# Kernel tuning notes

Measured on AMD Instinct MI355X. Metric: run time of the kernel, lower is better.

Reference implementation:

```python
import jax, jax.numpy as jnp
import numpy as np

ALPHA = 0.0005625
R_TIA = 0.1
DENOM = 2.0 * 1.5 * 0.025  # 2*n*VT = 0.075
V_D = 0.1
BN_EPS = 1e-5
KSZ, STRIDE, PAD = 3, 1, 1


def _unfold(x, k, s, p):
    # torch F.unfold equivalent: (N, C*k*k, L), channel-major then (ki, kj)
    N, C, H, W = x.shape
    Ho = (H + 2 * p - k) // s + 1
    Wo = (W + 2 * p - k) // s + 1
    xp = jnp.pad(x, ((0, 0), (0, 0), (p, p), (p, p)))
    cols = [xp[:, :, i:i + s * Ho:s, j:j + s * Wo:s]
            for i in range(k) for j in range(k)]  # each (N, C, Ho, Wo)
    patches = jnp.stack(cols, axis=2)             # (N, C, k*k, Ho, Wo)
    return patches.reshape(N, C * k * k, Ho * Wo), Ho, Wo


def setup_inputs() -> dict:
    key = jax.random.key(0)
    kx, kt = jax.random.split(key)
    x = jax.random.normal(kx, (32, 3, 32, 32), dtype=jnp.float32)
    theta = jax.random.uniform(kt, (3 * KSZ * KSZ, 64), dtype=jnp.float32,
                               minval=0.0, maxval=9.0)
    gamma = jnp.ones((64,), dtype=jnp.float32)
    beta = jnp.zeros((64,), dtype=jnp.float32)
    return {"x": x, "theta": theta, "gamma": gamma, "beta": beta}


def reference(x, theta, gamma, beta):
    N = x.shape[0]
    C_out = theta.shape[1]
    patches, Ho, Wo = _unfold(x, KSZ, STRIDE, PAD)      # (N, K, L)
    V_j = patches.transpose(0, 2, 1)[..., None]          # (N, L, K, 1)
    t1 = jax.nn.softplus((V_j - theta) / DENOM) ** 2     # (N, L, K, Cout)
    t2 = jax.nn.softplus((V_j - theta - V_D) / DENOM) ** 2
    I_k = ALPHA * jnp.sum(t1 - t2, axis=2)               # (N, L, Cout)
    V_out = (I_k * R_TIA).transpose(0, 2, 1).reshape(N, C_out, Ho, Wo)
    # BatchNorm2d in training mode: biased batch statistics
    mean = V_out.mean(axis=(0, 2, 3), keepdims=True)
    var = V_out.var(axis=(0, 2, 3), keepdims=True)
    V_hat = (V_out - mean) * jax.lax.rsqrt(var + BN_EPS)
    return V_hat * gamma[None, :, None, None] + beta[None, :, None, None]
```

## Files before the change

### kernel.cpp

```cpp
#include <hip/hip_runtime.h>


constexpr float INV_D  = 13.333333333333334f;
constexpr float C_NEG  = 0.2635971381157267f;
constexpr double OUT_SC = 5.625e-5 * 0.48045301391820142;
constexpr int   NCHUNK = 512;

__global__ __launch_bounds__(256)
void nlc_compute(const float* __restrict__ x, const float* __restrict__ theta,
                 float* __restrict__ vout, float* __restrict__ psum,
                 float* __restrict__ psq)
{
    __shared__ alignas(16) float thc[27 * 16];
    const int tid   = threadIdx.x;
    const int chunk = blockIdx.x >> 2;
    const int cbase = (blockIdx.x & 3) * 16;

    for (int i = tid; i < 27 * 16; i += 256) {
        const int k = i >> 4, cc = i & 15;
        thc[i] = __expf(-theta[k * 64 + cbase + cc] * INV_D);
    }
    __syncthreads();

    const int lane = tid & 63;
    const int wv   = tid >> 6;
    const int p    = chunk * 64 + lane;
    const int n    = p >> 10;
    const int hw   = p & 1023;
    const int h    = hw >> 5;
    const int w    = hw & 31;

    const float* xn = x + n * 3072;
    const float4* thv4 = reinterpret_cast<const float4*>(thc);

    int ad[9];
    unsigned okm = 0;
#pragma unroll
    for (int ki = 0; ki < 3; ++ki) {
#pragma unroll
        for (int kj = 0; kj < 3; ++kj) {
            const int  hh = h + ki - 1;
            const int  ww = w + kj - 1;
            const bool ok = ((unsigned)hh < 32u) & ((unsigned)ww < 32u);
            ad[ki * 3 + kj] = ok ? (hh * 32 + ww) : 0;
            okm |= (unsigned)ok << (ki * 3 + kj);
        }
    }

    float acc0 = 0.f, acc1 = 0.f, acc2 = 0.f, acc3 = 0.f;

#pragma unroll 1
    for (int ci = 0; ci < 3; ++ci) {
        float Ev[9];
#pragma unroll
        for (int j = 0; j < 9; ++j) {
            const float xv  = xn[ci * 1024 + ad[j]];
            const float val = ((okm >> j) & 1u) ? xv : 0.0f;
            Ev[j] = fminf(__expf(val * INV_D), 3.0e38f);
        }
#pragma unroll
        for (int j = 0; j < 9; ++j) {
            const float4 t4 = thv4[(ci * 9 + j) * 4 + wv];
            {
                const float E  = Ev[j] * t4.x;
                const float l1 = __log2f(1.0f + E);
                const float l2 = __log2f(fmaf(E, C_NEG, 1.0f));
                acc0 = fmaf(l1, l1, acc0);
                acc0 = fmaf(-l2, l2, acc0);
            }
            {
                const float E  = Ev[j] * t4.y;
                const float l1 = __log2f(1.0f + E);
                const float l2 = __log2f(fmaf(E, C_NEG, 1.0f));
                acc1 = fmaf(l1, l1, acc1);
                acc1 = fmaf(-l2, l2, acc1);
            }
            {
                const float E  = Ev[j] * t4.z;
                const float l1 = __log2f(1.0f + E);
                const float l2 = __log2f(fmaf(E, C_NEG, 1.0f));
                acc2 = fmaf(l1, l1, acc2);
                acc2 = fmaf(-l2, l2, acc2);
            }
            {
                const float E  = Ev[j] * t4.w;
                const float l1 = __log2f(1.0f + E);
                const float l2 = __log2f(fmaf(E, C_NEG, 1.0f));
                acc3 = fmaf(l1, l1, acc3);
                acc3 = fmaf(-l2, l2, acc3);
            }
        }
    }

    const float acc[4] = {acc0, acc1, acc2, acc3};
#pragma unroll
    for (int i = 0; i < 4; ++i) {
        const int   c  = cbase + wv * 4 + i;
        const float vo = acc[i];
        vout[(n << 16) + (c << 10) + hw] = vo;

        float s = vo, q = vo * vo;
#pragma unroll
        for (int off = 32; off > 0; off >>= 1) {
            s += __shfl_xor(s, off, 64);
            q += __shfl_xor(q, off, 64);
        }
        if (lane == 0) {
            psum[c * NCHUNK + chunk] = s;
            psq [c * NCHUNK + chunk] = q;
        }
    }
}

__global__ __launch_bounds__(256)
void nlc_finish(const float* __restrict__ psum, const float* __restrict__ psq,
                const float* __restrict__ gamma, const float* __restrict__ beta,
                float* __restrict__ vout)
{
    const int b   = blockIdx.x;
    const int c   = b >> 3;
    const int seg = b & 7;
    const int tid = threadIdx.x;

    float4* p0 = reinterpret_cast<float4*>(vout)
               + ((seg * 4 + 0) * 64 + c) * 256 + tid;
    float4* p1 = p0 + 64 * 256;
    float4* p2 = p1 + 64 * 256;
    float4* p3 = p2 + 64 * 256;
    float4 v0 = *p0, v1 = *p1, v2 = *p2, v3 = *p3;

    double s = (double)psum[c * NCHUNK + tid] + (double)psum[c * NCHUNK + 256 + tid];
    double q = (double)psq [c * NCHUNK + tid] + (double)psq [c * NCHUNK + 256 + tid];
#pragma unroll
    for (int off = 32; off > 0; off >>= 1) {
        s += __shfl_xor(s, off, 64);
        q += __shfl_xor(q, off, 64);
    }
    __shared__ double ls[4], lq[4];
    __shared__ float  scsh[2];
    if ((tid & 63) == 0) { ls[tid >> 6] = s; lq[tid >> 6] = q; }
    __syncthreads();
    if (tid == 0) {
        s = ls[0] + ls[1] + ls[2] + ls[3];
        q = lq[0] + lq[1] + lq[2] + lq[3];
        const double inv    = 1.0 / 32768.0;
        const double mean_a = s * inv;
        const double var_a  = q * inv - mean_a * mean_a;
        const double var_V  = var_a * OUT_SC * OUT_SC;
        const double rstd   = 1.0 / sqrt(var_V + 1e-5);
        const double sc     = (double)gamma[c] * rstd * OUT_SC;
        const double sh     = (double)beta[c] - mean_a * sc;
        scsh[0] = (float)sc;
        scsh[1] = (float)sh;
    }
    __syncthreads();
    const float sc = scsh[0];
    const float sh = scsh[1];

#define NLC_BN4(v) \
    v.x = fmaf(v.x, sc, sh); v.y = fmaf(v.y, sc, sh); \
    v.z = fmaf(v.z, sc, sh); v.w = fmaf(v.w, sc, sh);
    NLC_BN4(v0) NLC_BN4(v1) NLC_BN4(v2) NLC_BN4(v3)
#undef NLC_BN4

    *p0 = v0; *p1 = v1; *p2 = v2; *p3 = v3;
}

extern "C" void kernel_launch(void* const* d_in, const int* in_sizes, int n_in,
                              void* d_out, int out_size, void* d_ws, size_t ws_size,
                              hipStream_t stream)
{
    const float* x     = (const float*)d_in[0];
    const float* theta = (const float*)d_in[1];
    const float* gamma = (const float*)d_in[2];
    const float* beta  = (const float*)d_in[3];
    float* out = (float*)d_out;

    float* psum = (float*)d_ws;
    float* psq  = psum + 64 * NCHUNK;

    nlc_compute<<<NCHUNK * 4, 256, 0, stream>>>(x, theta, out, psum, psq);
    nlc_finish <<<512, 256, 0, stream>>>(psum, psq, gamma, beta, out);
}
```

Before: 33.79 us.

## Precompute input exponentials and use cubic series when whole wave has small E

Adds a small prepass kernel that computes exp(x/D) once per input element, so the conv kernel loads precomputed values instead of recomputing the exponential nine times per pixel. In the main loop, when every lane of a wave has E below a threshold, the two log2-squared terms are replaced by a cubic Taylor polynomial, skipping the transcendental calls. Theta in [0,9] makes E mostly tiny, so the fast branch should be taken often. The cost is an extra kernel launch, a workspace buffer, wave-uniform branches, and a small approximation error below the threshold.

```diff
diff --git a/kernel.cpp b/kernel.cpp
--- a/kernel.cpp
+++ b/kernel.cpp
@@ -2,12 +2,29 @@
 
 
 constexpr float INV_D  = 13.333333333333334f;
-constexpr float C_NEG  = 0.2635971381157267f;
-constexpr double OUT_SC = 5.625e-5 * 0.48045301391820142;
+constexpr double CD    = 0.26359713811572677;
+constexpr float C_NEG  = (float)CD;
+constexpr double LN2SQ = 0.4804530139182014;
+constexpr double OUT_SC = 5.625e-5 * LN2SQ;
+constexpr float TA = (float)((1.0 - CD * CD) / LN2SQ);
+constexpr float TB = (float)((1.0 - CD * CD * CD) / LN2SQ);
+constexpr float E_THR = 0.125f;
 constexpr int   NCHUNK = 512;
 
 __global__ __launch_bounds__(256)
-void nlc_compute(const float* __restrict__ x, const float* __restrict__ theta,
+void nlc_exp(const float* __restrict__ x, float* __restrict__ xe)
+{
+    const int i = blockIdx.x * 256 + threadIdx.x;
+    float4 v = reinterpret_cast<const float4*>(x)[i];
+    v.x = fminf(__expf(v.x * INV_D), 3.0e38f);
+    v.y = fminf(__expf(v.y * INV_D), 3.0e38f);
+    v.z = fminf(__expf(v.z * INV_D), 3.0e38f);
+    v.w = fminf(__expf(v.w * INV_D), 3.0e38f);
+    reinterpret_cast<float4*>(xe)[i] = v;
+}
+
+__global__ __launch_bounds__(256)
+void nlc_compute(const float* __restrict__ xe, const float* __restrict__ theta,
                  float* __restrict__ vout, float* __restrict__ psum,
                  float* __restrict__ psq)
 {
@@ -30,7 +47,7 @@
     const int h    = hw >> 5;
     const int w    = hw & 31;
 
-    const float* xn = x + n * 3072;
+    const float* xn = xe + n * 3072;
     const float4* thv4 = reinterpret_cast<const float4*>(thc);
 
     int ad[9];
@@ -54,38 +71,46 @@
         float Ev[9];
 #pragma unroll
         for (int j = 0; j < 9; ++j) {
-            const float xv  = xn[ci * 1024 + ad[j]];
-            const float val = ((okm >> j) & 1u) ? xv : 0.0f;
-            Ev[j] = fminf(__expf(val * INV_D), 3.0e38f);
+            const float ev = xn[ci * 1024 + ad[j]];
+            Ev[j] = ((okm >> j) & 1u) ? ev : 1.0f;
         }
 #pragma unroll
         for (int j = 0; j < 9; ++j) {
             const float4 t4 = thv4[(ci * 9 + j) * 4 + wv];
-            {
-                const float E  = Ev[j] * t4.x;
-                const float l1 = __log2f(1.0f + E);
-                const float l2 = __log2f(fmaf(E, C_NEG, 1.0f));
+            const float E0 = Ev[j] * t4.x;
+            const float E1 = Ev[j] * t4.y;
+            const float E2 = Ev[j] * t4.z;
+            const float E3 = Ev[j] * t4.w;
+
+            if (__all(E0 <= E_THR)) {
+                acc0 = fmaf(E0 * E0, fmaf(-TB, E0, TA), acc0);
+            } else {
+                const float l1 = __log2f(1.0f + E0);
+                const float l2 = __log2f(fmaf(E0, C_NEG, 1.0f));
                 acc0 = fmaf(l1, l1, acc0);
                 acc0 = fmaf(-l2, l2, acc0);
             }
-            {
-                const float E  = Ev[j] * t4.y;
-                const float l1 = __log2f(1.0f + E);
-                const float l2 = __log2f(fmaf(E, C_NEG, 1.0f));
+            if (__all(E1 <= E_THR)) {
+                acc1 = fmaf(E1 * E1, fmaf(-TB, E1, TA), acc1);
+            } else {
+                const float l1 = __log2f(1.0f + E1);
+                const float l2 = __log2f(fmaf(E1, C_NEG, 1.0f));
                 acc1 = fmaf(l1, l1, acc1);
                 acc1 = fmaf(-l2, l2, acc1);
             }
-            {
-                const float E  = Ev[j] * t4.z;
-                const float l1 = __log2f(1.0f + E);
-                const float l2 = __log2f(fmaf(E, C_NEG, 1.0f));
+            if (__all(E2 <= E_THR)) {
+                acc2 = fmaf(E2 * E2, fmaf(-TB, E2, TA), acc2);
+            } else {
+                const float l1 = __log2f(1.0f + E2);
+                const float l2 = __log2f(fmaf(E2, C_NEG, 1.0f));
                 acc2 = fmaf(l1, l1, acc2);
                 acc2 = fmaf(-l2, l2, acc2);
             }
-            {
-                const float E  = Ev[j] * t4.w;
-                const float l1 = __log2f(1.0f + E);
-                const float l2 = __log2f(fmaf(E, C_NEG, 1.0f));
+            if (__all(E3 <= E_THR)) {
+                acc3 = fmaf(E3 * E3, fmaf(-TB, E3, TA), acc3);
+            } else {
+                const float l1 = __log2f(1.0f + E3);
+                const float l2 = __log2f(fmaf(E3, C_NEG, 1.0f));
                 acc3 = fmaf(l1, l1, acc3);
                 acc3 = fmaf(-l2, l2, acc3);
             }
@@ -178,7 +203,9 @@
 
     float* psum = (float*)d_ws;
     float* psq  = psum + 64 * NCHUNK;
-
-    nlc_compute<<<NCHUNK * 4, 256, 0, stream>>>(x, theta, out, psum, psq);
+    float* xe   = psq  + 64 * NCHUNK;
+
+    nlc_exp    <<<96, 256, 0, stream>>>(x, xe);
+    nlc_compute<<<NCHUNK * 4, 256, 0, stream>>>(xe, theta, out, psum, psq);
     nlc_finish <<<512, 256, 0, stream>>>(psum, psq, gamma, beta, out);
 }
```

Measured after the change: 33.63 us. About the same (-0.5%).

## Precompute exp(x) and exp(-theta) in prepass kernels; two channels per wave

Applied to the files above, without the earlier changes.

Adds two small prepass kernels that compute exp(x/D) for the input and exp(-theta/D) per channel into workspace. The main kernel then loads these directly and reads theta terms as wave-uniform scalars, with no shared-memory staging or __syncthreads. Each wave now handles 2 channels instead of 4 and the grid doubles to 4096 blocks, so each block has less work and there is more parallelism. In exchange there are two extra kernel launches with their launch overhead, and each input exponential is computed once rather than once per channel group.

```diff
diff --git a/kernel.cpp b/kernel.cpp
--- a/kernel.cpp
+++ b/kernel.cpp
@@ -2,36 +2,55 @@
 
 
 constexpr float INV_D  = 13.333333333333334f;
-constexpr float C_NEG  = 0.2635971381157267f;
-constexpr double OUT_SC = 5.625e-5 * 0.48045301391820142;
+constexpr double CD    = 0.26359713811572677;
+constexpr float C_NEG  = (float)CD;
+constexpr double LN2SQ = 0.4804530139182014;
+constexpr double OUT_SC = 5.625e-5 * LN2SQ;
 constexpr int   NCHUNK = 512;
 
 __global__ __launch_bounds__(256)
-void nlc_compute(const float* __restrict__ x, const float* __restrict__ theta,
+void nlc_exp(const float* __restrict__ x, float* __restrict__ xe)
+{
+    const int i = blockIdx.x * 256 + threadIdx.x;
+    float4 v = reinterpret_cast<const float4*>(x)[i];
+    v.x = fminf(__expf(v.x * INV_D), 3.0e38f);
+    v.y = fminf(__expf(v.y * INV_D), 3.0e38f);
+    v.z = fminf(__expf(v.z * INV_D), 3.0e38f);
+    v.w = fminf(__expf(v.w * INV_D), 3.0e38f);
+    reinterpret_cast<float4*>(xe)[i] = v;
+}
+
+__global__ __launch_bounds__(256)
+void nlc_eth(const float* __restrict__ theta, float* __restrict__ eth)
+{
+    const int i = blockIdx.x * 256 + threadIdx.x;
+    const int c = i >> 5, k = i & 31;
+    if (k < 27)
+        eth[c * 32 + k] = __expf(-theta[k * 64 + c] * INV_D);
+}
+
+__global__ __launch_bounds__(256)
+void nlc_compute(const float* __restrict__ xe, const float* __restrict__ eth,
                  float* __restrict__ vout, float* __restrict__ psum,
                  float* __restrict__ psq)
 {
-    __shared__ alignas(16) float thc[27 * 16];
     const int tid   = threadIdx.x;
-    const int chunk = blockIdx.x >> 2;
-    const int cbase = (blockIdx.x & 3) * 16;
+    const int lane  = tid & 63;
+    const int W     = blockIdx.x * 4 + (tid >> 6);
+    const int chunk = W >> 5;
+    const int c0    = (W & 31) * 2;
 
-    for (int i = tid; i < 27 * 16; i += 256) {
-        const int k = i >> 4, cc = i & 15;
-        thc[i] = __expf(-theta[k * 64 + cbase + cc] * INV_D);
-    }
-    __syncthreads();
+    const int c0u = __builtin_amdgcn_readfirstlane(c0);
+    const float* th0 = eth + c0u * 32;
+    const float* th1 = th0 + 32;
 
-    const int lane = tid & 63;
-    const int wv   = tid >> 6;
-    const int p    = chunk * 64 + lane;
-    const int n    = p >> 10;
-    const int hw   = p & 1023;
-    const int h    = hw >> 5;
-    const int w    = hw & 31;
+    const int p  = chunk * 64 + lane;
+    const int n  = p >> 10;
+    const int hw = p & 1023;
+    const int h  = hw >> 5;
+    const int w  = hw & 31;
 
-    const float* xn = x + n * 3072;
-    const float4* thv4 = reinterpret_cast<const float4*>(thc);
+    const float* xn = xe + n * 3072;
 
     int ad[9];
     unsigned okm = 0;
@@ -47,55 +66,41 @@
         }
     }
 
-    float acc0 = 0.f, acc1 = 0.f, acc2 = 0.f, acc3 = 0.f;
+    float acc0 = 0.f, acc1 = 0.f;
 
 #pragma unroll 1
     for (int ci = 0; ci < 3; ++ci) {
         float Ev[9];
 #pragma unroll
         for (int j = 0; j < 9; ++j) {
-            const float xv  = xn[ci * 1024 + ad[j]];
-            const float val = ((okm >> j) & 1u) ? xv : 0.0f;
-            Ev[j] = fminf(__expf(val * INV_D), 3.0e38f);
+            const float ev = xn[ci * 1024 + ad[j]];
+            Ev[j] = ((okm >> j) & 1u) ? ev : 1.0f;
         }
 #pragma unroll
         for (int j = 0; j < 9; ++j) {
-            const float4 t4 = thv4[(ci * 9 + j) * 4 + wv];
+            const float s0 = th0[ci * 9 + j];
+            const float s1 = th1[ci * 9 + j];
             {
-                const float E  = Ev[j] * t4.x;
+                const float E  = Ev[j] * s0;
                 const float l1 = __log2f(1.0f + E);
                 const float l2 = __log2f(fmaf(E, C_NEG, 1.0f));
                 acc0 = fmaf(l1, l1, acc0);
                 acc0 = fmaf(-l2, l2, acc0);
             }
             {
-                const float E  = Ev[j] * t4.y;
+                const float E  = Ev[j] * s1;
                 const float l1 = __log2f(1.0f + E);
                 const float l2 = __log2f(fmaf(E, C_NEG, 1.0f));
                 acc1 = fmaf(l1, l1, acc1);
                 acc1 = fmaf(-l2, l2, acc1);
             }
-            {
-                const float E  = Ev[j] * t4.z;
-                const float l1 = __log2f(1.0f + E);
-                const float l2 = __log2f(fmaf(E, C_NEG, 1.0f));
-                acc2 = fmaf(l1, l1, acc2);
-                acc2 = fmaf(-l2, l2, acc2);
-            }
-            {
-                const float E  = Ev[j] * t4.w;
-                const float l1 = __log2f(1.0f + E);
-                const float l2 = __log2f(fmaf(E, C_NEG, 1.0f));
-                acc3 = fmaf(l1, l1, acc3);
-                acc3 = fmaf(-l2, l2, acc3);
-            }
         }
     }
 
-    const float acc[4] = {acc0, acc1, acc2, acc3};
+    const float acc[2] = {acc0, acc1};
 #pragma unroll
-    for (int i = 0; i < 4; ++i) {
-        const int   c  = cbase + wv * 4 + i;
+    for (int i = 0; i < 2; ++i) {
+        const int   c  = c0 + i;
         const float vo = acc[i];
         vout[(n << 16) + (c << 10) + hw] = vo;
 
@@ -178,7 +183,11 @@
 
     float* psum = (float*)d_ws;
     float* psq  = psum + 64 * NCHUNK;
+    float* xe   = psq  + 64 * NCHUNK;
+    float* eth  = xe   + 98304;
 
-    nlc_compute<<<NCHUNK * 4, 256, 0, stream>>>(x, theta, out, psum, psq);
+    nlc_exp    <<<96, 256, 0, stream>>>(x, xe);
+    nlc_eth    <<<8, 256, 0, stream>>>(theta, eth);
+    nlc_compute<<<4096, 256, 0, stream>>>(xe, eth, out, psum, psq);
     nlc_finish <<<512, 256, 0, stream>>>(psum, psq, gamma, beta, out);
 }
```

New measurement: 38.51 us. 1.14x slower.
